# Kernel tuning notes

Hardware: AMD Instinct MI355X
Metric: run time of the kernel (lower is better)

## Reference

```python
import jax, jax.numpy as jnp
import numpy as np

RADIUS = 0.1
NSAMPLE = 64
NEVENT = 2048
B, N, D = 4, 16384, 62
CHANNEL = D + 2  # 64


def index_events(events, idx):
    # events: [B, N, C], idx: [B, ...] -> [B, ..., C]
    return jax.vmap(lambda e, i: e[i])(events, idx)


def square_distance(src, dst):
    # src: [B, S, 2], dst: [B, N, 2] -> [B, S, N]
    return (jnp.sum(src ** 2, -1)[:, :, None]
            + jnp.sum(dst ** 2, -1)[:, None, :]
            - 2.0 * jnp.einsum('bsc,bnc->bsn', src, dst))


def research_circle(radius, nsample, xy, new_xy):
    n = xy.shape[1]
    sqrdists = square_distance(new_xy, xy)            # [B, S, N]
    ar = jnp.arange(n, dtype=jnp.int32)
    group_idx = jnp.where(sqrdists > radius ** 2, n, ar)  # out-of-ball -> N (sorts last)
    group_idx = jnp.sort(group_idx, axis=-1)[:, :, :nsample]
    first = group_idx[:, :, :1]
    return jnp.where(group_idx == n, first, group_idx)     # [B, S, nsample]


def reference(xy, events, fps_idx, affine_alpha, affine_beta):
    b, _, c = xy.shape
    new_xy = index_events(xy, fps_idx)                     # [B, S, 2]
    idx = research_circle(RADIUS, NSAMPLE, xy, new_xy)     # [B, S, K]
    grouped_xy = index_events(xy, idx)                     # [B, S, K, 2]
    grouped_events = index_events(events, idx)             # [B, S, K, D]
    # Normalize (normalize='center')
    g = jnp.concatenate([grouped_events, grouped_xy], axis=-1)  # [B, S, K, D+2]
    mean = jnp.mean(g, axis=2, keepdims=True)              # [B, S, 1, C]
    centered = g - mean
    std = jnp.std(centered.reshape(b, -1), axis=-1, ddof=1)[:, None, None, None]
    g = centered / (std + 1e-05)
    new_events = affine_alpha * g + affine_beta            # [B, S, K, 64]
    return new_xy, new_events


def setup_inputs() -> dict:
    key = jax.random.key(0)
    k1, k2, k3 = jax.random.split(key, 3)
    xy = jax.random.uniform(k1, (B, N, 2), dtype=jnp.float32)
    events = jax.random.normal(k2, (B, N, D), dtype=jnp.float32)
    fps_idx = jax.random.randint(k3, (B, NEVENT), 0, N, dtype=jnp.int32)
    affine_alpha = jnp.ones((1, 1, 1, CHANNEL), dtype=jnp.float32)
    affine_beta = jnp.zeros((1, 1, 1, CHANNEL), dtype=jnp.float32)
    return {"xy": xy, "events": events, "fps_idx": fps_idx,
            "affine_alpha": affine_alpha, "affine_beta": affine_beta}
```

## Files before the change

### kernel.cpp

```cpp
#include <hip/hip_runtime.h>
#include <stdint.h>
#include <math.h>

#define NPTS 16384
#define DEV 62
#define NEVENT 2048
#define NSAMPLE 64
#define CH 64
#define NBATCH 4
#define STOT (NBATCH * NEVENT)
#define M_PER_BATCH (NEVENT * NSAMPLE * CH)

#define OUT1_BASE 16384
#define REG_STRIDE (NSAMPLE * CH)
#define SL_MEAN 64
#define SL_INV 128
#define SL_SS 129

__device__ __forceinline__ int swz_query8192(int blk) {
    int x = blk & 7;
    int j = blk >> 3;
    return (x & 3) * NEVENT + (x >> 2) * (NEVENT / 2) + j;
}
__device__ __forceinline__ int swz_group2048(int blk) {
    int x = blk & 7;
    int j = blk >> 3;
    return (x & 3) * (NEVENT / 4) + (x >> 2) * (NEVENT / 8) + j;
}

__global__ __launch_bounds__(256) void knn_kernel(
    const float2* __restrict__ xy,
    const int* __restrict__ fps,
    float* __restrict__ out)
{
    int grp  = swz_group2048(blockIdx.x);
    int wave = grp * 4 + (threadIdx.x >> 6);
    int lane = threadIdx.x & 63;
    int b = wave >> 11;

    const float2* xyb = xy + b * NPTS;
    int qi = fps[wave];
    float2 q = xyb[qi];
    if (lane == 0) ((float2*)out)[wave] = q;

    float ssq = __fadd_rn(__fmul_rn(q.x, q.x), __fmul_rn(q.y, q.y));
    const float thr = 0.01f;

    int* regidx = (int*)(out + OUT1_BASE + (size_t)wave * REG_STRIDE);
    int m = 0;
    int first = -1;

    for (int base = 0; base < NPTS; base += 256) {
        float2 p0 = xyb[base       + lane];
        float2 p1 = xyb[base +  64 + lane];
        float2 p2 = xyb[base + 128 + lane];
        float2 p3 = xyb[base + 192 + lane];

        auto proc = [&](float2 p, int idxbase) {
            float ssp = __fadd_rn(__fmul_rn(p.x, p.x), __fmul_rn(p.y, p.y));
            float dot = __builtin_fmaf(q.y, p.y, __fmul_rn(q.x, p.x));
            float d   = __fsub_rn(__fadd_rn(ssq, ssp), __fmul_rn(2.0f, dot));
            bool ok = !(d > thr);
            unsigned long long bal = __ballot(ok);
            if (first < 0 && bal != 0ull)
                first = idxbase + (__ffsll((unsigned long long)bal) - 1);
            if (ok) {
                int pos = m + __popcll(bal & ((1ull << lane) - 1ull));
                if (pos < NSAMPLE) regidx[pos] = idxbase + lane;
            }
            m += __popcll(bal);
        };
        proc(p0, base);
        proc(p1, base + 64);
        proc(p2, base + 128);
        proc(p3, base + 192);
        if (m >= NSAMPLE) break;
    }
    if (m < NSAMPLE) {
        for (int p = m + lane; p < NSAMPLE; p += 64)
            regidx[p] = first;
    }
}

__global__ __launch_bounds__(256) void stats_kernel(
    const float2* __restrict__ xy,
    const float* __restrict__ ev,
    float* __restrict__ out)
{
    int s = swz_query8192(blockIdx.x);
    int b = s >> 11;
    int tid = threadIdx.x;
    float* reg = out + OUT1_BASE + (size_t)s * REG_STRIDE;

    __shared__ int sidx[NSAMPLE];
    __shared__ float ssum[2][256];
    __shared__ float smean[CH];
    __shared__ float swred[4];

    if (tid < NSAMPLE) sidx[tid] = ((const int*)reg)[tid];
    __syncthreads();

    int c2 = tid & 31;
    int kq = tid >> 5;

    const float* evb = ev + (size_t)b * NPTS * DEV;
    const float2* xyb = xy + b * NPTS;

    float g0[8], g1[8];
    float a0 = 0.f, a1 = 0.f;
#pragma unroll
    for (int j = 0; j < 8; ++j) {
        int row = sidx[8 * j + kq];
        float2 v;
        if (c2 < 31) v = *(const float2*)(evb + (size_t)row * DEV + 2 * c2);
        else         v = xyb[row];
        g0[j] = v.x; g1[j] = v.y;
        a0 += v.x;   a1 += v.y;
    }
    ssum[0][tid] = a0;
    ssum[1][tid] = a1;
    __syncthreads();

    if (tid < CH) {
        int which = tid >> 5, cc = tid & 31;
        float t = 0.f;
#pragma unroll
        for (int q = 0; q < 8; ++q) t += ssum[which][q * 32 + cc];
        smean[2 * cc + which] = t * (1.0f / NSAMPLE);
    }
    __syncthreads();

    if (tid < CH) reg[SL_MEAN + tid] = smean[tid];

    float m0 = smean[2 * c2], m1 = smean[2 * c2 + 1];
    float ss = 0.f;
#pragma unroll
    for (int j = 0; j < 8; ++j) {
        float c0 = g0[j] - m0;
        float c1 = g1[j] - m1;
        ss += c0 * c0 + c1 * c1;
    }

    for (int off = 32; off > 0; off >>= 1) ss += __shfl_down(ss, off, 64);
    if ((tid & 63) == 0) swred[tid >> 6] = ss;
    __syncthreads();
    if (tid == 0) reg[SL_SS] = swred[0] + swred[1] + swred[2] + swred[3];
}

__global__ __launch_bounds__(256) void reduce_std_kernel(float* __restrict__ out)
{
    int b = blockIdx.x;
    int tid = threadIdx.x;
    double acc = 0.0;
    for (int i = tid; i < NEVENT; i += 256)
        acc += (double)out[OUT1_BASE + (size_t)(b * NEVENT + i) * REG_STRIDE + SL_SS];
    __shared__ double sd[256];
    __shared__ float sinv;
    sd[tid] = acc;
    __syncthreads();
    for (int off = 128; off > 0; off >>= 1) {
        if (tid < off) sd[tid] += sd[tid + off];
        __syncthreads();
    }
    if (tid == 0) {
        double stdv = sqrt(sd[0] / (double)(M_PER_BATCH - 1));
        sinv = (float)(1.0 / (stdv + 1e-5));
    }
    __syncthreads();
    float inv = sinv;
    for (int i = tid; i < NEVENT; i += 256)
        out[OUT1_BASE + (size_t)(b * NEVENT + i) * REG_STRIDE + SL_INV] = inv;
}

__global__ __launch_bounds__(256) void finalize_kernel(
    const float2* __restrict__ xy,
    const float* __restrict__ ev,
    const float* __restrict__ alpha,
    const float* __restrict__ beta,
    float* __restrict__ out)
{
    int s = swz_query8192(blockIdx.x);
    int b = s >> 11;
    int tid = threadIdx.x;
    float* reg = out + OUT1_BASE + (size_t)s * REG_STRIDE;

    __shared__ int sidx[NSAMPLE];
    __shared__ float sm[CH], sa[CH], sbet[CH];
    __shared__ float sinv;

    if (tid < NSAMPLE) {
        sidx[tid] = ((const int*)reg)[tid];
        sm[tid] = reg[SL_MEAN + tid];
    } else if (tid < 128) {
        sa[tid - 64] = alpha[tid - 64];
        sbet[tid - 64] = beta[tid - 64];
    } else if (tid == 128) {
        sinv = reg[SL_INV];
    }
    __syncthreads();

    int c2 = tid & 31;
    int kq = tid >> 5;
    float inv = sinv;

    const float* evb = ev + (size_t)b * NPTS * DEV;
    const float2* xyb = xy + b * NPTS;

    float m0 = sm[2 * c2],   m1 = sm[2 * c2 + 1];
    float al0 = sa[2 * c2],  al1 = sa[2 * c2 + 1];
    float be0 = sbet[2 * c2], be1 = sbet[2 * c2 + 1];

    float2* outp = (float2*)reg;
#pragma unroll
    for (int j = 0; j < 8; ++j) {
        int row = sidx[8 * j + kq];
        float2 v;
        if (c2 < 31) v = *(const float2*)(evb + (size_t)row * DEV + 2 * c2);
        else         v = xyb[row];
        float2 r;
        r.x = al0 * ((v.x - m0) * inv) + be0;
        r.y = al1 * ((v.y - m1) * inv) + be1;
        outp[256 * j + tid] = r;
    }
}

extern "C" void kernel_launch(void* const* d_in, const int* in_sizes, int n_in,
                              void* d_out, int out_size, void* d_ws, size_t ws_size,
                              hipStream_t stream) {
    const float2* xy    = (const float2*)d_in[0];
    const float*  ev    = (const float*)d_in[1];
    const int*    fps   = (const int*)d_in[2];
    const float*  alpha = (const float*)d_in[3];
    const float*  beta  = (const float*)d_in[4];
    float* out = (float*)d_out;
    (void)d_ws; (void)ws_size;

    knn_kernel<<<STOT / 4, 256, 0, stream>>>(xy, fps, out);
    stats_kernel<<<STOT, 256, 0, stream>>>(xy, ev, out);
    reduce_std_kernel<<<NBATCH, 256, 0, stream>>>(out);
    finalize_kernel<<<STOT, 256, 0, stream>>>(xy, ev, alpha, beta, out);
}
```

Measured before the change: 195.4 us.

## Fuse ball-query and per-group stats into one kernel via shared index staging

Merges the kNN ball-query kernel and the per-query mean/sum-of-squares kernel into a single launch. Each wave's selected indices are also written to shared memory, so after a block barrier the whole block computes statistics for its four queries without re-reading indices from global memory. This removes one kernel launch and the global round trip for indices. In exchange, stats work is serialized over four queries per block with extra barriers, and there are fewer blocks (2048 instead of 8192) for the gather phase, which may reduce latency hiding.

```diff
diff --git a/kernel.cpp b/kernel.cpp
--- a/kernel.cpp
+++ b/kernel.cpp
@@ -28,15 +28,22 @@
     return (x & 3) * (NEVENT / 4) + (x >> 2) * (NEVENT / 8) + j;
 }
 
-__global__ __launch_bounds__(256) void knn_kernel(
+__global__ __launch_bounds__(256) void knn_stats_kernel(
     const float2* __restrict__ xy,
+    const float* __restrict__ ev,
     const int* __restrict__ fps,
     float* __restrict__ out)
 {
     int grp  = swz_group2048(blockIdx.x);
-    int wave = grp * 4 + (threadIdx.x >> 6);
+    int w    = threadIdx.x >> 6;
     int lane = threadIdx.x & 63;
-    int b = wave >> 11;
+    int wave = grp * 4 + w;
+    int b    = grp >> 9;
+
+    __shared__ int   sidx[4][NSAMPLE];
+    __shared__ float ssum[2][256];
+    __shared__ float smean[CH];
+    __shared__ float swred[4];
 
     const float2* xyb = xy + b * NPTS;
     int qi = fps[wave];
@@ -66,7 +73,10 @@
                 first = idxbase + (__ffsll((unsigned long long)bal) - 1);
             if (ok) {
                 int pos = m + __popcll(bal & ((1ull << lane) - 1ull));
-                if (pos < NSAMPLE) regidx[pos] = idxbase + lane;
+                if (pos < NSAMPLE) {
+                    regidx[pos]  = idxbase + lane;
+                    sidx[w][pos] = idxbase + lane;
+                }
             }
             m += __popcll(bal);
         };
@@ -77,74 +87,64 @@
         if (m >= NSAMPLE) break;
     }
     if (m < NSAMPLE) {
-        for (int p = m + lane; p < NSAMPLE; p += 64)
-            regidx[p] = first;
-    }
-}
-
-__global__ __launch_bounds__(256) void stats_kernel(
-    const float2* __restrict__ xy,
-    const float* __restrict__ ev,
-    float* __restrict__ out)
-{
-    int s = swz_query8192(blockIdx.x);
-    int b = s >> 11;
+        for (int p = m + lane; p < NSAMPLE; p += 64) {
+            regidx[p]  = first;
+            sidx[w][p] = first;
+        }
+    }
+
+    __syncthreads();
+
     int tid = threadIdx.x;
-    float* reg = out + OUT1_BASE + (size_t)s * REG_STRIDE;
-
-    __shared__ int sidx[NSAMPLE];
-    __shared__ float ssum[2][256];
-    __shared__ float smean[CH];
-    __shared__ float swred[4];
-
-    if (tid < NSAMPLE) sidx[tid] = ((const int*)reg)[tid];
-    __syncthreads();
-
     int c2 = tid & 31;
     int kq = tid >> 5;
-
     const float* evb = ev + (size_t)b * NPTS * DEV;
-    const float2* xyb = xy + b * NPTS;
-
-    float g0[8], g1[8];
-    float a0 = 0.f, a1 = 0.f;
-#pragma unroll
-    for (int j = 0; j < 8; ++j) {
-        int row = sidx[8 * j + kq];
-        float2 v;
-        if (c2 < 31) v = *(const float2*)(evb + (size_t)row * DEV + 2 * c2);
-        else         v = xyb[row];
-        g0[j] = v.x; g1[j] = v.y;
-        a0 += v.x;   a1 += v.y;
-    }
-    ssum[0][tid] = a0;
-    ssum[1][tid] = a1;
-    __syncthreads();
-
-    if (tid < CH) {
-        int which = tid >> 5, cc = tid & 31;
-        float t = 0.f;
-#pragma unroll
-        for (int q = 0; q < 8; ++q) t += ssum[which][q * 32 + cc];
-        smean[2 * cc + which] = t * (1.0f / NSAMPLE);
-    }
-    __syncthreads();
-
-    if (tid < CH) reg[SL_MEAN + tid] = smean[tid];
-
-    float m0 = smean[2 * c2], m1 = smean[2 * c2 + 1];
-    float ss = 0.f;
-#pragma unroll
-    for (int j = 0; j < 8; ++j) {
-        float c0 = g0[j] - m0;
-        float c1 = g1[j] - m1;
-        ss += c0 * c0 + c1 * c1;
-    }
-
-    for (int off = 32; off > 0; off >>= 1) ss += __shfl_down(ss, off, 64);
-    if ((tid & 63) == 0) swred[tid >> 6] = ss;
-    __syncthreads();
-    if (tid == 0) reg[SL_SS] = swred[0] + swred[1] + swred[2] + swred[3];
+
+    for (int qq = 0; qq < 4; ++qq) {
+        int s = grp * 4 + qq;
+        float* reg = out + OUT1_BASE + (size_t)s * REG_STRIDE;
+
+        float g0[8], g1[8];
+        float a0 = 0.f, a1 = 0.f;
+#pragma unroll
+        for (int j = 0; j < 8; ++j) {
+            int row = sidx[qq][8 * j + kq];
+            float2 v;
+            if (c2 < 31) v = *(const float2*)(evb + (size_t)row * DEV + 2 * c2);
+            else         v = xyb[row];
+            g0[j] = v.x; g1[j] = v.y;
+            a0 += v.x;   a1 += v.y;
+        }
+        ssum[0][tid] = a0;
+        ssum[1][tid] = a1;
+        __syncthreads();
+
+        if (tid < CH) {
+            int which = tid >> 5, cc = tid & 31;
+            float t = 0.f;
+#pragma unroll
+            for (int p = 0; p < 8; ++p) t += ssum[which][p * 32 + cc];
+            smean[2 * cc + which] = t * (1.0f / NSAMPLE);
+        }
+        __syncthreads();
+
+        if (tid < CH) reg[SL_MEAN + tid] = smean[tid];
+
+        float m0 = smean[2 * c2], m1 = smean[2 * c2 + 1];
+        float ss = 0.f;
+#pragma unroll
+        for (int j = 0; j < 8; ++j) {
+            float c0 = g0[j] - m0;
+            float c1 = g1[j] - m1;
+            ss += c0 * c0 + c1 * c1;
+        }
+
+        for (int off = 32; off > 0; off >>= 1) ss += __shfl_down(ss, off, 64);
+        if ((tid & 63) == 0) swred[tid >> 6] = ss;
+        __syncthreads();
+        if (tid == 0) reg[SL_SS] = swred[0] + swred[1] + swred[2] + swred[3];
+        __syncthreads();
+    }
 }
 
 __global__ __launch_bounds__(256) void reduce_std_kernel(float* __restrict__ out)
@@ -235,8 +235,7 @@
     float* out = (float*)d_out;
     (void)d_ws; (void)ws_size;
 
-    knn_kernel<<<STOT / 4, 256, 0, stream>>>(xy, fps, out);
-    stats_kernel<<<STOT, 256, 0, stream>>>(xy, ev, out);
+    knn_stats_kernel<<<STOT / 4, 256, 0, stream>>>(xy, ev, fps, out);
     reduce_std_kernel<<<NBATCH, 256, 0, stream>>>(out);
     finalize_kernel<<<STOT, 256, 0, stream>>>(xy, ev, alpha, beta, out);
 }
```

Result: no change. 193.8 us (median of 2 runs) (-0.8%).
